# Kernel optimization log

Hardware: AMD Instinct MI355X
Metric: run time of the kernel (lower is better)

The kernel has to match this reference:

```python
import jax, jax.numpy as jnp
import numpy as np

B, S, H = 4, 2048, 1024
NH, NKV, HD = 16, 4, 64
EPS = 1e-6
SCALE = 1.0 / np.sqrt(HD)
N_REP = NH // NKV


def setup_inputs() -> dict:
    key = jax.random.key(0)
    ks = jax.random.split(key, 8)
    hidden_states = jax.random.normal(ks[0], (B, S, H), dtype=jnp.float32)
    # additive causal mask [1,1,S,S]: 0 on/below diagonal, -1e9 above
    causal_mask = jnp.where(
        jnp.tril(jnp.ones((S, S), dtype=bool)), 0.0, -1e9
    ).astype(jnp.float32)[None, None]
    # interleaved RoPE tables [S, HD] (each frequency repeated twice, matching _rotate_half's even/odd split)
    inv_freq = 1.0 / (10000.0 ** (np.arange(0, HD, 2, dtype=np.float32) / HD))
    angles = jnp.arange(S, dtype=jnp.float32)[:, None] * jnp.asarray(inv_freq)[None, :]
    emb = jnp.repeat(angles, 2, axis=-1)  # [S, HD]
    cos, sin = jnp.cos(emb), jnp.sin(emb)
    # learned params (stored [in, out] for einsum)
    Wq = jax.random.normal(ks[1], (H, NH * HD), dtype=jnp.float32) * 0.02
    Wk = jax.random.normal(ks[2], (H, NKV * HD), dtype=jnp.float32) * 0.02
    Wv = jax.random.normal(ks[3], (H, NKV * HD), dtype=jnp.float32) * 0.02
    Wo = jax.random.normal(ks[4], (NH * HD, H), dtype=jnp.float32) * 0.02
    q_norm_w = jnp.ones((HD,), dtype=jnp.float32)
    k_norm_w = jnp.ones((HD,), dtype=jnp.float32)
    return {"hidden_states": hidden_states, "causal_mask": causal_mask, "cos": cos,
            "sin": sin, "Wq": Wq, "Wk": Wk, "Wv": Wv, "Wo": Wo,
            "q_norm_w": q_norm_w, "k_norm_w": k_norm_w}


def _rms_norm(x, w):
    var = jnp.mean(jnp.square(x), axis=-1, keepdims=True)
    return x * jax.lax.rsqrt(var + EPS) * w


def _rotate_half(x):
    x1 = x[..., ::2]
    x2 = x[..., 1::2]
    return jnp.stack((-x2, x1), axis=-1).reshape(x.shape)


def reference(hidden_states, causal_mask, cos, sin, Wq, Wk, Wv, Wo, q_norm_w, k_norm_w):
    b, s, _ = hidden_states.shape
    q = jnp.einsum('bsh,hd->bsd', hidden_states, Wq).reshape(b, s, NH, HD)
    k = jnp.einsum('bsh,hd->bsd', hidden_states, Wk).reshape(b, s, NKV, HD)
    v = jnp.einsum('bsh,hd->bsd', hidden_states, Wv).reshape(b, s, NKV, HD)
    q = _rms_norm(q, q_norm_w)
    k = _rms_norm(k, k_norm_w)
    q = q.transpose(0, 2, 1, 3)  # [b, NH, s, HD]
    k = k.transpose(0, 2, 1, 3)  # [b, NKV, s, HD]
    v = v.transpose(0, 2, 1, 3)
    c = cos[None, None]  # [1,1,s,HD]
    sn = sin[None, None]
    q = q * c + _rotate_half(q) * sn
    k = k * c + _rotate_half(k) * sn
    if N_REP > 1:
        k = jnp.repeat(k, N_REP, axis=1)  # GQA expand -> [b, NH, s, HD]
        v = jnp.repeat(v, N_REP, axis=1)
    scores = jnp.einsum('bhqd,bhkd->bhqk', q, k) * SCALE + causal_mask
    probs = jax.nn.softmax(scores, axis=-1)
    attn = jnp.einsum('bhqk,bhkd->bhqd', probs, v)
    attn = attn.transpose(0, 2, 1, 3).reshape(b, s, NH * HD)
    return jnp.einsum('bsd,dh->bsh', attn, Wo)
```

## Files before the change

### kernel.cpp

```cpp
#include <hip/hip_runtime.h>

typedef unsigned short u16;
typedef unsigned int u32;

typedef __attribute__((ext_vector_type(8))) short bf16x8;
typedef __attribute__((ext_vector_type(4))) float f32x4;

#define QSCALE 0.18033688011112042f

__device__ __forceinline__ u16 f2bf(float x) {
    union { float f; u32 u; } v; v.f = x;
    u32 r = (v.u + 0x7FFFu + ((v.u >> 16) & 1u)) >> 16;
    return (u16)r;
}
__device__ __forceinline__ float bf2f(u16 x) {
    union { u32 u; float f; } v; v.u = ((u32)x) << 16;
    return v.f;
}
__device__ __forceinline__ u32 pk2(float x, float y) {
    u32 ax = __float_as_uint(x) + 0x8000u;
    u32 ay = __float_as_uint(y) + 0x8000u;
    return __builtin_amdgcn_perm(ay, ax, 0x07060302u);
}

__device__ __forceinline__ void cp16(const u16* g, u16* l) {
    __builtin_amdgcn_global_load_lds(
        (__attribute__((address_space(1))) void*)(g),
        (__attribute__((address_space(3))) void*)(l), 16, 0, 0);
}

__global__ void k_prep(const float* __restrict__ hidden, u16* __restrict__ hA,
                       const float* __restrict__ Wq, u16* __restrict__ WqT,
                       const float* __restrict__ Wk, u16* __restrict__ WkT,
                       const float* __restrict__ Wv, u16* __restrict__ WvT,
                       const float* __restrict__ Wo, u16* __restrict__ WoT) {
    __shared__ u16 t[64][72];
    int bid = blockIdx.x, tid = threadIdx.x;
    if (bid < 4096) {
        int i = (bid * 256 + tid) * 8;
        float4 a = *(const float4*)(hidden + i);
        float4 b = *(const float4*)(hidden + i + 4);
        ushort4 o0; o0.x = f2bf(a.x); o0.y = f2bf(a.y); o0.z = f2bf(a.z); o0.w = f2bf(a.w);
        ushort4 o1; o1.x = f2bf(b.x); o1.y = f2bf(b.y); o1.z = f2bf(b.z); o1.w = f2bf(b.w);
        *(ushort4*)(hA + i) = o0;
        *(ushort4*)(hA + i + 4) = o1;
        return;
    }
    int rb = bid - 4096;
    const float* W; u16* Wt; int N, bx, by;
    if (rb < 256)      { W = Wq; Wt = WqT; N = 1024; bx = rb & 15; by = rb >> 4; }
    else if (rb < 320) { W = Wk; Wt = WkT; N = 256;  rb -= 256; bx = rb & 3; by = rb >> 2; }
    else if (rb < 384) { W = Wv; Wt = WvT; N = 256;  rb -= 320; bx = rb & 3; by = rb >> 2; }
    else               { W = Wo; Wt = WoT; N = 1024; rb -= 384; bx = rb & 15; by = rb >> 4; }
    const int K = 1024;
    int rr = tid >> 2;
    int cs = tid & 3;
    const float* src = W + (by*64 + rr)*N + bx*64 + cs*16;
#pragma unroll
    for (int j = 0; j < 16; j += 4) {
        float4 v = *(const float4*)(src + j);
        t[rr][cs*16 + j + 0] = f2bf(v.x);
        t[rr][cs*16 + j + 1] = f2bf(v.y);
        t[rr][cs*16 + j + 2] = f2bf(v.z);
        t[rr][cs*16 + j + 3] = f2bf(v.w);
    }
    __syncthreads();
    u16* dst = Wt + (bx*64 + rr)*K + by*64 + cs*16;
#pragma unroll
    for (int j = 0; j < 16; ++j) dst[j] = t[cs*16 + j][rr];
}

__device__ __forceinline__ void stage_ab(const u16* __restrict__ Asrc, const u16* __restrict__ Bsrc,
                                         int kt, u16* At, u16* Bt, int tid, int wv) {
#pragma unroll
    for (int i = 0; i < 2; ++i) {
        int q = i*256 + tid;
        int r = q >> 2, sidx = q & 3;
        int s = sidx ^ ((r >> 1) & 3);
        cp16(Asrc + r*1024 + kt*32 + s*8, At + (i*256 + wv*64)*8);
        cp16(Bsrc + r*1024 + kt*32 + s*8, Bt + (i*256 + wv*64)*8);
    }
}

__global__ __launch_bounds__(256) void k_gemm(
    const u16* __restrict__ A,
    const u16* __restrict__ Bq, const u16* __restrict__ Bk, const u16* __restrict__ Bv,
    float* __restrict__ outF,
    u16* __restrict__ outQ, u16* __restrict__ outK, u16* __restrict__ outV,
    int mode)
{
    __shared__ __align__(16) u16 At[2][128*32];
    __shared__ __align__(16) u16 Bt[2][128*32];
    int tid = threadIdx.x;
    int lane = tid & 63, wv = tid >> 6;
    int l15 = lane & 15, quad = lane >> 4;
    int wm = wv >> 1, wn = wv & 1;
    int mb = blockIdx.x, nb = blockIdx.y;

    const u16* Bsrc; int target; int colLocal0;
    if (mode == 0)      { Bsrc = Bq + nb*128*1024;      target = 3; colLocal0 = nb*128; }
    else if (nb < 8)    { Bsrc = Bq + nb*128*1024;      target = 0; colLocal0 = nb*128; }
    else if (nb < 10)   { Bsrc = Bk + (nb-8)*128*1024;  target = 1; colLocal0 = (nb-8)*128; }
    else                { Bsrc = Bv + (nb-10)*128*1024; target = 2; colLocal0 = (nb-10)*128; }
    const u16* Asrc = A + mb*128*1024;

    f32x4 zf = {0.f, 0.f, 0.f, 0.f};
    f32x4 acc[4][4];
#pragma unroll
    for (int i = 0; i < 4; ++i)
#pragma unroll
        for (int j = 0; j < 4; ++j) acc[i][j] = zf;

    stage_ab(Asrc, Bsrc, 0, At[0], Bt[0], tid, wv);
    __syncthreads();

    for (int kt = 0; kt < 32; ++kt) {
        int cur = kt & 1;
        if (kt < 31) stage_ab(Asrc, Bsrc, kt + 1, At[cur ^ 1], Bt[cur ^ 1], tid, wv);
        bf16x8 af[4], bfr[4];
#pragma unroll
        for (int mt = 0; mt < 4; ++mt) {
            int row = wm*64 + mt*16 + l15;
            int sidx = quad ^ ((row >> 1) & 3);
            af[mt] = *(const bf16x8*)(At[cur] + row*32 + sidx*8);
        }
#pragma unroll
        for (int nt = 0; nt < 4; ++nt) {
            int row = wn*64 + nt*16 + l15;
            int sidx = quad ^ ((row >> 1) & 3);
            bfr[nt] = *(const bf16x8*)(Bt[cur] + row*32 + sidx*8);
        }
#pragma unroll
        for (int mt = 0; mt < 4; ++mt)
#pragma unroll
            for (int nt = 0; nt < 4; ++nt)
                acc[mt][nt] = __builtin_amdgcn_mfma_f32_16x16x32_bf16(af[mt], bfr[nt], acc[mt][nt], 0, 0, 0);
        __syncthreads();
    }

#pragma unroll
    for (int mt = 0; mt < 4; ++mt) {
#pragma unroll
        for (int nt = 0; nt < 4; ++nt) {
#pragma unroll
            for (int rr = 0; rr < 4; ++rr) {
                int row = mb*128 + wm*64 + mt*16 + quad*4 + rr;
                int cl  = colLocal0 + wn*64 + nt*16 + l15;
                float v = acc[mt][nt][rr];
                if (target == 3) {
                    outF[row*1024 + cl] = v;
                } else {
                    int b = row >> 11, s = row & 2047;
                    int hh = cl >> 6, d = cl & 63;
                    u16 bv = f2bf(v);
                    if (target == 0)      outQ[((b*16 + hh)*2048 + s)*64 + d] = bv;
                    else if (target == 1) outK[((b*4  + hh)*2048 + s)*64 + d] = bv;
                    else                  outV[((b*4  + hh)*2048 + s)*64 + d] = bv;
                }
            }
        }
    }
}

__global__ void k_nv(u16* __restrict__ Q, u16* __restrict__ K,
                     const float* __restrict__ qw, const float* __restrict__ kw,
                     const float* __restrict__ cosp, const float* __restrict__ sinp,
                     const u16* __restrict__ V, u16* __restrict__ VT)
{
    __shared__ u16 t[64][72];
    int bid = blockIdx.x, tid = threadIdx.x;
    if (bid < 20480) {
        int row = bid * 8 + (tid >> 5);
        int tl = tid & 31;
        u16* base; const float* w; int s; float post;
        if (row < 131072) { base = Q + row*64; s = row & 2047; w = qw; post = QSCALE; }
        else { int r2 = row - 131072; base = K + r2*64; s = r2 & 2047; w = kw; post = 1.0f; }
        u32 packed = *(const u32*)(base + 2*tl);
        float x0 = bf2f((u16)(packed & 0xffffu));
        float x1 = bf2f((u16)(packed >> 16));
        float ss = x0*x0 + x1*x1;
#pragma unroll
        for (int m = 1; m < 32; m <<= 1) ss += __shfl_xor(ss, m, 32);
        float inv = rsqrtf(ss * (1.0f/64.0f) + 1e-6f);
        float w0 = w[2*tl], w1 = w[2*tl+1];
        float c = cosp[s*64 + 2*tl], sn = sinp[s*64 + 2*tl];
        float xn0 = x0 * inv * w0, xn1 = x1 * inv * w1;
        float y0 = (xn0*c - xn1*sn) * post;
        float y1 = (xn1*c + xn0*sn) * post;
        *(u32*)(base + 2*tl) = pk2(y0, y1);
        return;
    }
    int idx = bid - 20480;
    int sb = idx & 31, bh = idx >> 5;
    int r = tid >> 2, cs = tid & 3;
    const u16* src = V + (bh*2048 + sb*64 + r)*64 + cs*16;
    uint4 v0 = *(const uint4*)(src);
    uint4 v1 = *(const uint4*)(src + 8);
    *(uint4*)&t[r][cs*16]     = v0;
    *(uint4*)&t[r][cs*16 + 8] = v1;
    __syncthreads();
    u16* dst = VT + (bh*64 + r)*2048 + sb*64 + cs*16;
#pragma unroll
    for (int j = 0; j < 16; ++j) dst[j] = t[cs*16 + j][r];
}

__device__ __forceinline__ void stage_kv(const u16* __restrict__ Kg, const u16* __restrict__ Vg,
                                         int kt, u16* sK, u16* sV, int tid, int wv) {
#pragma unroll
    for (int i = 0; i < 2; ++i) {
        int q = i*256 + tid;
        int r = q >> 3, sidx = q & 7;
        int s = sidx ^ (r & 7);
        cp16(Kg + (kt*64 + r)*64 + s*8, sK + (i*256 + wv*64)*8);
        cp16(Vg + r*2048 + kt*64 + s*8, sV + (i*256 + wv*64)*8);
    }
}

__global__ __launch_bounds__(256, 4) void k_attn(
    const u16* __restrict__ Q, const u16* __restrict__ K,
    const u16* __restrict__ VT, u16* __restrict__ attn)
{
    __shared__ __align__(16) u16 smemP[64*64];
    __shared__ __align__(16) u16 smemK[64*64];
    __shared__ __align__(16) u16 smemV[64*64];

    int tid = threadIdx.x;
    int lane = tid & 63, wv = tid >> 6;
    int l15 = lane & 15, quad = lane >> 4;
    int p = blockIdx.x;
    int h = blockIdx.y, b = blockIdx.z;
    const u16* Kg = K + ((b*4 + (h >> 2))*2048)*64;
    const u16* Vg = VT + (b*4 + (h >> 2))*64*2048;

    int qcol = wv*16 + l15;

#pragma unroll
    for (int t = 0; t < 2; ++t) {
        int qi = t ? p : (31 - p);
        int q0 = qi * 64;
        const u16* Qg = Q + ((b*16 + h)*2048 + q0)*64;

        bf16x8 qf[2];
#pragma unroll
        for (int ks = 0; ks < 2; ++ks)
            qf[ks] = *(const bf16x8*)(Qg + (wv*16 + l15)*64 + ks*32 + quad*8);

        f32x4 zf = {0.f, 0.f, 0.f, 0.f};
        f32x4 o[4];
#pragma unroll
        for (int mt = 0; mt < 4; ++mt) o[mt] = zf;
        float l_q = 0.f;
        int qrow = q0 + wv*16 + l15;

        for (int kt = 0; kt <= qi; ++kt) {
            stage_kv(Kg, Vg, kt, smemK, smemV, tid, wv);
            __syncthreads();

            f32x4 sc[4];
#pragma unroll
            for (int mt = 0; mt < 4; ++mt) sc[mt] = zf;
#pragma unroll
            for (int ks = 0; ks < 2; ++ks) {
                bf16x8 kf[4];
#pragma unroll
                for (int mt = 0; mt < 4; ++mt) {
                    int row = mt*16 + l15;
                    int sidx = (ks*4 + quad) ^ (row & 7);
                    kf[mt] = *(const bf16x8*)(smemK + row*64 + sidx*8);
                }
#pragma unroll
                for (int mt = 0; mt < 4; ++mt)
                    sc[mt] = __builtin_amdgcn_mfma_f32_16x16x32_bf16(kf[mt], qf[ks], sc[mt], 0, 0, 0);
            }

            if (kt == qi) {
                int keyb = kt*64 + quad*4;
#pragma unroll
                for (int mt = 0; mt < 4; ++mt)
#pragma unroll
                    for (int r = 0; r < 4; ++r)
                        if (keyb + mt*16 + r > qrow) sc[mt][r] = -1e30f;
            }
            float rs = 0.f;
#pragma unroll
            for (int mt = 0; mt < 4; ++mt) {
                float p0 = __builtin_amdgcn_exp2f(sc[mt][0]);
                float p1 = __builtin_amdgcn_exp2f(sc[mt][1]);
                float p2 = __builtin_amdgcn_exp2f(sc[mt][2]);
                float p3 = __builtin_amdgcn_exp2f(sc[mt][3]);
                rs += (p0 + p1) + (p2 + p3);
                uint2 w; w.x = pk2(p0, p1); w.y = pk2(p2, p3);
                int gw = (mt*2 + (quad >> 1)) ^ (qcol & 7);
                *(uint2*)(smemP + qcol*64 + gw*8 + (quad & 1)*4) = w;
            }
            l_q += rs;

#pragma unroll
            for (int ks2 = 0; ks2 < 2; ++ks2) {
                int gr = (ks2*4 + quad) ^ (qcol & 7);
                bf16x8 pf = *(const bf16x8*)(smemP + qcol*64 + gr*8);
                bf16x8 vf[4];
#pragma unroll
                for (int mt = 0; mt < 4; ++mt) {
                    int row = mt*16 + l15;
                    int sidx = (ks2*4 + quad) ^ (row & 7);
                    vf[mt] = *(const bf16x8*)(smemV + row*64 + sidx*8);
                }
#pragma unroll
                for (int mt = 0; mt < 4; ++mt)
                    o[mt] = __builtin_amdgcn_mfma_f32_16x16x32_bf16(vf[mt], pf, o[mt], 0, 0, 0);
            }
            __syncthreads();
        }

        float lt = l_q;
        lt += __shfl_xor(lt, 16);
        lt += __shfl_xor(lt, 32);
        float rl = 1.0f / lt;
#pragma unroll
        for (int mt = 0; mt < 4; ++mt) {
            uint2 w;
            w.x = pk2(o[mt][0]*rl, o[mt][1]*rl);
            w.y = pk2(o[mt][2]*rl, o[mt][3]*rl);
            int gw = (mt*2 + (quad >> 1)) ^ (qcol & 7);
            *(uint2*)(smemP + qcol*64 + gw*8 + (quad & 1)*4) = w;
        }
        __syncthreads();
        {
            int r2 = tid >> 2, c = tid & 3;
            u16* dst = attn + (b*2048 + q0 + r2)*1024 + h*64 + c*16;
            int g0 = (c*2) ^ (r2 & 7);
            int g1 = (c*2 + 1) ^ (r2 & 7);
            *(uint4*)(dst)     = *(const uint4*)(smemP + r2*64 + g0*8);
            *(uint4*)(dst + 8) = *(const uint4*)(smemP + r2*64 + g1*8);
        }
        __syncthreads();
    }
}

extern "C" void kernel_launch(void* const* d_in, const int* in_sizes, int n_in,
                              void* d_out, int out_size, void* d_ws, size_t ws_size,
                              hipStream_t stream) {
    const float* hidden = (const float*)d_in[0];
    const float* cosp = (const float*)d_in[2];
    const float* sinp = (const float*)d_in[3];
    const float* Wq = (const float*)d_in[4];
    const float* Wk = (const float*)d_in[5];
    const float* Wv = (const float*)d_in[6];
    const float* Wo = (const float*)d_in[7];
    const float* qw = (const float*)d_in[8];
    const float* kw = (const float*)d_in[9];
    float* out = (float*)d_out;

    char* ws = (char*)d_ws;
    u16* hA   = (u16*)(ws);
    u16* WqT  = (u16*)(ws + 16777216);
    u16* WkT  = (u16*)(ws + 18874368);
    u16* WvT  = (u16*)(ws + 19398656);
    u16* WoT  = (u16*)(ws + 19922944);
    u16* Qws  = (u16*)(ws + 22020096);
    u16* Kws  = (u16*)(ws + 38797312);
    u16* Vws  = (u16*)(ws + 42991616);
    u16* VTw  = (u16*)(ws + 47185920);
    u16* attn = hA;

    k_prep<<<4736, 256, 0, stream>>>(hidden, hA, Wq, WqT, Wk, WkT, Wv, WvT, Wo, WoT);
    k_gemm<<<dim3(64, 12), 256, 0, stream>>>(hA, WqT, WkT, WvT, nullptr, Qws, Kws, Vws, 1);
    k_nv<<<20992, 256, 0, stream>>>(Qws, Kws, qw, kw, cosp, sinp, Vws, VTw);
    k_attn<<<dim3(16, 16, 4), 256, 0, stream>>>(Qws, Kws, VTw, attn);
    k_gemm<<<dim3(64, 8), 256, 0, stream>>>(attn, WoT, nullptr, nullptr, out, nullptr, nullptr, nullptr, 0);
}
```

Before: 246.3 us.

## Fuse V transpose into QKV GEMM epilogue and Q norm/RoPE into attention

```diff
diff --git a/kernel.cpp b/kernel.cpp
--- a/kernel.cpp
+++ b/kernel.cpp
@@ -86,11 +86,12 @@
     const u16* __restrict__ A,
     const u16* __restrict__ Bq, const u16* __restrict__ Bk, const u16* __restrict__ Bv,
     float* __restrict__ outF,
-    u16* __restrict__ outQ, u16* __restrict__ outK, u16* __restrict__ outV,
+    u16* __restrict__ outQ, u16* __restrict__ outK, u16* __restrict__ outVT,
     int mode)
 {
-    __shared__ __align__(16) u16 At[2][128*32];
-    __shared__ __align__(16) u16 Bt[2][128*32];
+    __shared__ __align__(16) u16 smem[16384];
+    u16* At0 = smem;
+    u16* Bt0 = smem + 8192;
     int tid = threadIdx.x;
     int lane = tid & 63, wv = tid >> 6;
     int l15 = lane & 15, quad = lane >> 4;
@@ -111,24 +112,24 @@
 #pragma unroll
         for (int j = 0; j < 4; ++j) acc[i][j] = zf;
 
-    stage_ab(Asrc, Bsrc, 0, At[0], Bt[0], tid, wv);
+    stage_ab(Asrc, Bsrc, 0, At0, Bt0, tid, wv);
     __syncthreads();
 
     for (int kt = 0; kt < 32; ++kt) {
         int cur = kt & 1;
-        if (kt < 31) stage_ab(Asrc, Bsrc, kt + 1, At[cur ^ 1], Bt[cur ^ 1], tid, wv);
+        if (kt < 31) stage_ab(Asrc, Bsrc, kt + 1, At0 + (cur^1)*4096, Bt0 + (cur^1)*4096, tid, wv);
         bf16x8 af[4], bfr[4];
 #pragma unroll
         for (int mt = 0; mt < 4; ++mt) {
             int row = wm*64 + mt*16 + l15;
             int sidx = quad ^ ((row >> 1) & 3);
-            af[mt] = *(const bf16x8*)(At[cur] + row*32 + sidx*8);
+            af[mt] = *(const bf16x8*)(At0 + cur*4096 + row*32 + sidx*8);
         }
 #pragma unroll
         for (int nt = 0; nt < 4; ++nt) {
             int row = wn*64 + nt*16 + l15;
             int sidx = quad ^ ((row >> 1) & 3);
-            bfr[nt] = *(const bf16x8*)(Bt[cur] + row*32 + sidx*8);
+            bfr[nt] = *(const bf16x8*)(Bt0 + cur*4096 + row*32 + sidx*8);
         }
 #pragma unroll
         for (int mt = 0; mt < 4; ++mt)
@@ -136,6 +137,39 @@
             for (int nt = 0; nt < 4; ++nt)
                 acc[mt][nt] = __builtin_amdgcn_mfma_f32_16x16x32_bf16(af[mt], bfr[nt], acc[mt][nt], 0, 0, 0);
         __syncthreads();
+    }
+
+    if (target == 2) {
+#pragma unroll
+        for (int mt = 0; mt < 4; ++mt) {
+#pragma unroll
+            for (int nt = 0; nt < 4; ++nt) {
+                int cl_local = wn*64 + nt*16 + l15;
+                int rowb = wm*64 + mt*16 + quad*4;
+                int g = rowb >> 3;
+                int sub = (rowb & 7) * 2;
+                int gp = g ^ (cl_local & 15);
+                uint2 w2;
+                w2.x = pk2(acc[mt][nt][0], acc[mt][nt][1]);
+                w2.y = pk2(acc[mt][nt][2], acc[mt][nt][3]);
+                *(uint2*)((char*)(smem + cl_local*128) + gp*16 + sub) = w2;
+            }
+        }
+        __syncthreads();
+        int row0 = mb*128;
+        int b = row0 >> 11, s0 = row0 & 2047;
+        int dl = tid >> 1, half = tid & 1;
+        int cl = colLocal0 + dl;
+        int hh = cl >> 6, d = cl & 63;
+        u16* dst = outVT + ((b*4 + hh)*64 + d)*2048 + s0 + half*64;
+#pragma unroll
+        for (int j = 0; j < 8; ++j) {
+            int g = half*8 + j;
+            int gp = g ^ (dl & 15);
+            uint4 vv = *(const uint4*)((const char*)(smem + dl*128) + gp*16);
+            *(uint4*)(dst + j*8) = vv;
+        }
+        return;
     }
 
 #pragma unroll
@@ -154,54 +188,34 @@
                     int hh = cl >> 6, d = cl & 63;
                     u16 bv = f2bf(v);
                     if (target == 0)      outQ[((b*16 + hh)*2048 + s)*64 + d] = bv;
-                    else if (target == 1) outK[((b*4  + hh)*2048 + s)*64 + d] = bv;
-                    else                  outV[((b*4  + hh)*2048 + s)*64 + d] = bv;
+                    else                  outK[((b*4  + hh)*2048 + s)*64 + d] = bv;
                 }
             }
         }
     }
 }
 
-__global__ void k_nv(u16* __restrict__ Q, u16* __restrict__ K,
-                     const float* __restrict__ qw, const float* __restrict__ kw,
-                     const float* __restrict__ cosp, const float* __restrict__ sinp,
-                     const u16* __restrict__ V, u16* __restrict__ VT)
+__global__ void k_knorm(u16* __restrict__ K,
+                        const float* __restrict__ kw,
+                        const float* __restrict__ cosp, const float* __restrict__ sinp)
 {
-    __shared__ u16 t[64][72];
-    int bid = blockIdx.x, tid = threadIdx.x;
-    if (bid < 20480) {
-        int row = bid * 8 + (tid >> 5);
-        int tl = tid & 31;
-        u16* base; const float* w; int s; float post;
-        if (row < 131072) { base = Q + row*64; s = row & 2047; w = qw; post = QSCALE; }
-        else { int r2 = row - 131072; base = K + r2*64; s = r2 & 2047; w = kw; post = 1.0f; }
-        u32 packed = *(const u32*)(base + 2*tl);
-        float x0 = bf2f((u16)(packed & 0xffffu));
-        float x1 = bf2f((u16)(packed >> 16));
-        float ss = x0*x0 + x1*x1;
-#pragma unroll
-        for (int m = 1; m < 32; m <<= 1) ss += __shfl_xor(ss, m, 32);
-        float inv = rsqrtf(ss * (1.0f/64.0f) + 1e-6f);
-        float w0 = w[2*tl], w1 = w[2*tl+1];
-        float c = cosp[s*64 + 2*tl], sn = sinp[s*64 + 2*tl];
-        float xn0 = x0 * inv * w0, xn1 = x1 * inv * w1;
-        float y0 = (xn0*c - xn1*sn) * post;
-        float y1 = (xn1*c + xn0*sn) * post;
-        *(u32*)(base + 2*tl) = pk2(y0, y1);
-        return;
-    }
-    int idx = bid - 20480;
-    int sb = idx & 31, bh = idx >> 5;
-    int r = tid >> 2, cs = tid & 3;
-    const u16* src = V + (bh*2048 + sb*64 + r)*64 + cs*16;
-    uint4 v0 = *(const uint4*)(src);
-    uint4 v1 = *(const uint4*)(src + 8);
-    *(uint4*)&t[r][cs*16]     = v0;
-    *(uint4*)&t[r][cs*16 + 8] = v1;
-    __syncthreads();
-    u16* dst = VT + (bh*64 + r)*2048 + sb*64 + cs*16;
-#pragma unroll
-    for (int j = 0; j < 16; ++j) dst[j] = t[cs*16 + j][r];
+    int row = blockIdx.x * 8 + (threadIdx.x >> 5);
+    int tl = threadIdx.x & 31;
+    u16* base = K + row*64;
+    int s = row & 2047;
+    u32 packed = *(const u32*)(base + 2*tl);
+    float x0 = bf2f((u16)(packed & 0xffffu));
+    float x1 = bf2f((u16)(packed >> 16));
+    float ss = x0*x0 + x1*x1;
+#pragma unroll
+    for (int m = 1; m < 32; m <<= 1) ss += __shfl_xor(ss, m, 32);
+    float inv = rsqrtf(ss * (1.0f/64.0f) + 1e-6f);
+    float w0 = kw[2*tl], w1 = kw[2*tl+1];
+    float c = cosp[s*64 + 2*tl], sn = sinp[s*64 + 2*tl];
+    float xn0 = x0 * inv * w0, xn1 = x1 * inv * w1;
+    float y0 = xn0*c - xn1*sn;
+    float y1 = xn1*c + xn0*sn;
+    *(u32*)(base + 2*tl) = pk2(y0, y1);
 }
 
 __device__ __forceinline__ void stage_kv(const u16* __restrict__ Kg, const u16* __restrict__ Vg,
@@ -218,7 +232,9 @@
 
 __global__ __launch_bounds__(256, 4) void k_attn(
     const u16* __restrict__ Q, const u16* __restrict__ K,
-    const u16* __restrict__ VT, u16* __restrict__ attn)
+    const u16* __restrict__ VT, u16* __restrict__ attn,
+    const float* __restrict__ qw,
+    const float* __restrict__ cosp, const float* __restrict__ sinp)
 {
     __shared__ __align__(16) u16 smemP[64*64];
     __shared__ __align__(16) u16 smemK[64*64];
@@ -227,10 +243,17 @@
     int tid = threadIdx.x;
     int lane = tid & 63, wv = tid >> 6;
     int l15 = lane & 15, quad = lane >> 4;
-    int p = blockIdx.x;
-    int h = blockIdx.y, b = blockIdx.z;
-    const u16* Kg = K + ((b*4 + (h >> 2))*2048)*64;
-    const u16* Vg = VT + (b*4 + (h >> 2))*64*2048;
+
+    int bid = blockIdx.x;
+    int r8 = bid & 7, q8 = bid >> 3;
+    int g = ((q8 >> 6) << 3) | r8;
+    int local = q8 & 63;
+    int b = g >> 2, hkv = g & 3;
+    int hl = local >> 4, p = local & 15;
+    int h = hkv*4 + hl;
+
+    const u16* Kg = K + ((b*4 + hkv)*2048)*64;
+    const u16* Vg = VT + (b*4 + hkv)*64*2048;
 
     int qcol = wv*16 + l15;
 
@@ -239,18 +262,55 @@
         int qi = t ? p : (31 - p);
         int q0 = qi * 64;
         const u16* Qg = Q + ((b*16 + h)*2048 + q0)*64;
+        int qrow = q0 + qcol;
 
         bf16x8 qf[2];
-#pragma unroll
-        for (int ks = 0; ks < 2; ++ks)
-            qf[ks] = *(const bf16x8*)(Qg + (wv*16 + l15)*64 + ks*32 + quad*8);
+        {
+            float xv[2][8];
+            float ssum = 0.f;
+#pragma unroll
+            for (int ks = 0; ks < 2; ++ks) {
+                bf16x8 raw = *(const bf16x8*)(Qg + qcol*64 + ks*32 + quad*8);
+#pragma unroll
+                for (int j = 0; j < 8; ++j) {
+                    float x = bf2f((u16)raw[j]);
+                    xv[ks][j] = x;
+                    ssum += x*x;
+                }
+            }
+            ssum += __shfl_xor(ssum, 16);
+            ssum += __shfl_xor(ssum, 32);
+            float inv = rsqrtf(ssum * (1.0f/64.0f) + 1e-6f);
+#pragma unroll
+            for (int ks = 0; ks < 2; ++ks) {
+                int d0 = ks*32 + quad*8;
+                float4 w0 = *(const float4*)(qw + d0);
+                float4 w1 = *(const float4*)(qw + d0 + 4);
+                float4 c0 = *(const float4*)(cosp + qrow*64 + d0);
+                float4 c1 = *(const float4*)(cosp + qrow*64 + d0 + 4);
+                float4 s0 = *(const float4*)(sinp + qrow*64 + d0);
+                float4 s1 = *(const float4*)(sinp + qrow*64 + d0 + 4);
+                float wa[8] = {w0.x,w0.y,w0.z,w0.w,w1.x,w1.y,w1.z,w1.w};
+                float ca[8] = {c0.x,c0.y,c0.z,c0.w,c1.x,c1.y,c1.z,c1.w};
+                float sa[8] = {s0.x,s0.y,s0.z,s0.w,s1.x,s1.y,s1.z,s1.w};
+                union { u32 u[4]; bf16x8 v; } qq;
+#pragma unroll
+                for (int jj = 0; jj < 4; ++jj) {
+                    float xe = xv[ks][2*jj]   * inv * wa[2*jj];
+                    float xo = xv[ks][2*jj+1] * inv * wa[2*jj+1];
+                    float ye = (xe*ca[2*jj]   - xo*sa[2*jj])   * QSCALE;
+                    float yo = (xo*ca[2*jj+1] + xe*sa[2*jj+1]) * QSCALE;
+                    qq.u[jj] = pk2(ye, yo);
+                }
+                qf[ks] = qq.v;
+            }
+        }
 
         f32x4 zf = {0.f, 0.f, 0.f, 0.f};
         f32x4 o[4];
 #pragma unroll
         for (int mt = 0; mt < 4; ++mt) o[mt] = zf;
         float l_q = 0.f;
-        int qrow = q0 + wv*16 + l15;
 
         for (int kt = 0; kt <= qi; ++kt) {
             stage_kv(Kg, Vg, kt, smemK, smemV, tid, wv);
@@ -278,8 +338,8 @@
 #pragma unroll
                 for (int mt = 0; mt < 4; ++mt)
 #pragma unroll
-                    for (int r = 0; r < 4; ++r)
-                        if (keyb + mt*16 + r > qrow) sc[mt][r] = -1e30f;
+                    for (int rr = 0; rr < 4; ++rr)
+                        if (keyb + mt*16 + rr > qrow) sc[mt][rr] = -1e30f;
             }
             float rs = 0.f;
 #pragma unroll
@@ -360,13 +420,12 @@
     u16* WoT  = (u16*)(ws + 19922944);
     u16* Qws  = (u16*)(ws + 22020096);
     u16* Kws  = (u16*)(ws + 38797312);
-    u16* Vws  = (u16*)(ws + 42991616);
-    u16* VTw  = (u16*)(ws + 47185920);
+    u16* VTw  = (u16*)(ws + 42991616);
     u16* attn = hA;
 
     k_prep<<<4736, 256, 0, stream>>>(hidden, hA, Wq, WqT, Wk, WkT, Wv, WvT, Wo, WoT);
-    k_gemm<<<dim3(64, 12), 256, 0, stream>>>(hA, WqT, WkT, WvT, nullptr, Qws, Kws, Vws, 1);
-    k_nv<<<20992, 256, 0, stream>>>(Qws, Kws, qw, kw, cosp, sinp, Vws, VTw);
-    k_attn<<<dim3(16, 16, 4), 256, 0, stream>>>(Qws, Kws, VTw, attn);
+    k_gemm<<<dim3(64, 12), 256, 0, stream>>>(hA, WqT, WkT, WvT, nullptr, Qws, Kws, VTw, 1);
+    k_knorm<<<4096, 256, 0, stream>>>(Kws, kw, cosp, sinp);
+    k_attn<<<1024, 256, 0, stream>>>(Qws, Kws, VTw, attn, qw, cosp, sinp);
     k_gemm<<<dim3(64, 8), 256, 0, stream>>>(attn, WoT, nullptr, nullptr, out, nullptr, nullptr, nullptr, 0);
 }
```

After: 246.8 us. No clear change (+0.2%).
